# Kernel optimization log

Measured on AMD Instinct MI355X. Metric: run time of the kernel, lower is better.

Reference implementation:

```python
import jax, jax.numpy as jnp
import numpy as np

# MLABlock dims (from __init__ defaults / chosen init_kwargs)
B, S, D = 2, 2048, 2048
H = 16
NOPE, ROPE, VD = 128, 64, 128
KVR = 512
NE, TOPK = 12, 4
EI, SEI = 1024, 2048
THETA = 10000.0
MSCALE = 1.0
EPS = 1e-6


def setup_inputs() -> dict:
    key = jax.random.key(0)
    ks = jax.random.split(key, 14)
    w = lambda k, shp: jax.random.normal(k, shp, jnp.float32) * 0.02
    return {
        "x": jax.random.normal(ks[0], (B, S, D), jnp.float32),
        "start_pos": 0,
        "norm_w": jnp.ones((D,), jnp.float32),
        "wq": w(ks[1], (H * (NOPE + ROPE), D)),
        "wkv_a": w(ks[2], (KVR + ROPE, D)),
        "kv_norm_w": jnp.ones((KVR,), jnp.float32),
        "wkv_b": w(ks[3], (H * (NOPE + VD), KVR)),
        "wo": w(ks[4], (D, H * VD)),
        "gate_w": w(ks[5], (NE, D)),
        "gate_bias": w(ks[6], (NE,)),
        "w1": w(ks[7], (NE, EI, D)),
        "w2": w(ks[8], (NE, D, EI)),
        "w3": w(ks[9], (NE, EI, D)),
        "sw1": w(ks[10], (SEI, D)),
        "sw2": w(ks[11], (D, SEI)),
        "sw3": w(ks[12], (SEI, D)),
    }


def _rms(v, w):
    return v * jax.lax.rsqrt(jnp.mean(v * v, -1, keepdims=True) + EPS) * w


def reference(x, start_pos, norm_w, wq, wkv_a, kv_norm_w, wkv_b, wo,
              gate_w, gate_bias, w1, w2, w3, sw1, sw2, sw3):
    b, s, d = x.shape
    # ---- MLA attention sub-layer ----
    h = _rms(x, norm_w)
    q = (h @ wq.T).reshape(b, s, H, NOPE + ROPE)
    q_nope, q_pe = q[..., :NOPE], q[..., NOPE:]
    kv = h @ wkv_a.T                      # [b,s,KVR+ROPE]
    kv_lat, k_pe = kv[..., :KVR], kv[..., KVR:]
    # rotary embedding (interleaved pairs), positions start_pos..start_pos+s
    pos = jnp.arange(s, dtype=jnp.float32) + start_pos
    inv = 1.0 / (THETA ** (jnp.arange(0, ROPE, 2, dtype=jnp.float32) / ROPE))
    ang = pos[:, None] * inv              # [s, ROPE/2]
    cos = jnp.cos(ang)[None, :, None, :]
    sin = jnp.sin(ang)[None, :, None, :]
    def rot(t):                           # t: [b,s,h,ROPE]
        t1, t2 = t[..., 0::2], t[..., 1::2]
        return jnp.stack([t1 * cos - t2 * sin, t1 * sin + t2 * cos], -1).reshape(t.shape)
    q_pe = rot(q_pe)
    k_pe = rot(k_pe[:, :, None, :])       # [b,s,1,ROPE] shared across heads
    kv_lat = _rms(kv_lat, kv_norm_w)
    kvb = (kv_lat @ wkv_b.T).reshape(b, s, H, NOPE + VD)
    k_nope, v = kvb[..., :NOPE], kvb[..., NOPE:]
    k = jnp.concatenate([k_nope, jnp.broadcast_to(k_pe, (b, s, H, ROPE))], -1)
    qf = jnp.concatenate([q_nope, q_pe], -1)
    scale = MSCALE * (NOPE + ROPE) ** -0.5
    mask = jnp.triu(jnp.full((s, s), -1e9, x.dtype), 1)  # causal
    scores = jnp.einsum('bqhd,bkhd->bhqk', qf, k) * scale + mask
    attn = jax.nn.softmax(scores, -1)
    o = jnp.einsum('bhqk,bkhd->bqhd', attn, v).reshape(b, s, H * VD) @ wo.T
    first = o + x
    # ---- MoE sub-layer (shared self.norm reused) ----
    h2 = _rms(first, norm_w)
    g_scores = jax.nn.sigmoid(h2 @ gate_w.T)             # [b,s,NE]
    _, idx = jax.lax.top_k(g_scores + gate_bias, TOPK)   # adaptive-bias selection
    gw = jnp.take_along_axis(g_scores, idx, -1)          # weights from raw scores
    gw = gw / jnp.sum(gw, -1, keepdims=True)
    out = (jax.nn.silu(h2 @ sw1.T) * (h2 @ sw3.T)) @ sw2.T  # shared expert
    for e in range(NE):                                  # fixed small expert set
        we = jnp.sum(jnp.where(idx == e, gw, 0.0), -1)   # [b,s]
        ye = (jax.nn.silu(h2 @ w1[e].T) * (h2 @ w3[e].T)) @ w2[e].T
        out = out + we[..., None] * ye
    return out + first
```

## Files before the change

kernel.cpp:

```cpp
#include <hip/hip_runtime.h>
#include <cstdint>
#include <cstddef>
#include <cmath>

#define DI __device__ __forceinline__
typedef float f32x4 __attribute__((ext_vector_type(4)));
typedef __bf16 bf16x8 __attribute__((ext_vector_type(8)));
typedef unsigned short u16;
typedef unsigned int u32;

static constexpr int TKN = 4096, SEQ = 2048, DIM = 2048, NH = 16;

DI u16 f2bf(float f) {
  union { float f; u32 u; } v; v.f = f;
  u32 r = v.u + 0x7fffu + ((v.u >> 16) & 1u);
  return (u16)(r >> 16);
}
DI float bf2f(u16 h) {
  union { u32 u; float f; } v; v.u = ((u32)h) << 16;
  return v.f;
}
DI f32x4 mfma16(bf16x8 a, bf16x8 b, f32x4 c) {
  return __builtin_amdgcn_mfma_f32_16x16x32_bf16(a, b, c, 0, 0, 0);
}
DI void gld16(const u16* g, u16* l) {
  __builtin_amdgcn_global_load_lds((const __attribute__((address_space(1))) u32*)g,
                                   (__attribute__((address_space(3))) u32*)l, 16, 0, 0);
}

enum { EF_F32 = 0, EF_BF16 = 1, EF_RES = 2, EF_KV = 3, EF_SILU = 4, EF_ATOM = 5, EF_QROPE = 6 };
enum { AM_DIR = 0, AM_LIST = 1, AM_OFF = 2 };

template<int EPI, int AMODE, int NSEG>
__global__ __launch_bounds__(256)
void gemm_f(const u16* __restrict__ A, const u16* __restrict__ B, void* __restrict__ C,
            int M, int N, int K, size_t apl, size_t bpl,
            const int* __restrict__ list, const int* __restrict__ basep,
            const int* __restrict__ counts,
            const void* __restrict__ aux, const float* __restrict__ gws,
            u16* __restrict__ kd0, u16* __restrict__ kd1, u16* __restrict__ vT,
            const float* __restrict__ cosT)
{
  constexpr int BM = 128, BK = 64;
  __shared__ __align__(16) u16 As[BM * BK];
  __shared__ __align__(16) u16 Bs[BM * BK];
  int rowbase = 0;
  if (AMODE != AM_DIR) {
    int z = blockIdx.z;
    M = counts[z];
    rowbase = basep[z];
    B += (size_t)z * (size_t)N * K;
  }
  int m0 = blockIdx.x * BM, n0 = blockIdx.y * BM;
  if (m0 >= M) return;
  int tid = threadIdx.x, lane = tid & 63, wid = tid >> 6;
  int wm = (wid >> 1) * 64, wn = (wid & 1) * 64;
  int lr = lane & 15, lk = (lane >> 4) * 8;

  const u16* asrc[4];
  const u16* bsrc[4];
  int l8 = lane >> 3, c8 = ((lane & 7) ^ l8) * 8;
  #pragma unroll
  for (int i = 0; i < 4; i++) {
    int chunk = wid * 4 + i;
    int ra = m0 + chunk * 8 + l8;
    size_t rowidx;
    if (AMODE == AM_LIST)      rowidx = (size_t)list[rowbase + (ra < M ? ra : 0)];
    else if (AMODE == AM_OFF)  rowidx = (size_t)(rowbase + (ra < M ? ra : 0));
    else                       rowidx = (size_t)ra;
    asrc[i] = A + rowidx * (size_t)K + c8;
    int rb = n0 + chunk * 8 + l8;
    if (rb >= N) rb = N - 1;
    bsrc[i] = B + (size_t)rb * K + c8;
  }

  f32x4 acc[4][4] = {};
  int sw = lr & 7;
  #pragma unroll 1
  for (int s = 0; s < NSEG; s++) {
    int sa = (s == 4) ? 2 : (s & 1);
    int sb = (s == 5) ? 2 : ((s >> 1) & 1);
    size_t ao = (size_t)sa * apl, bo = (size_t)sb * bpl;
    for (int kt = 0; kt < K; kt += BK) {
      #pragma unroll
      for (int i = 0; i < 4; i++) {
        gld16(asrc[i] + ao + kt, &As[(wid * 4 + i) * 512]);
        gld16(bsrc[i] + bo + kt, &Bs[(wid * 4 + i) * 512]);
      }
      __syncthreads();
      #pragma unroll
      for (int ko = 0; ko < BK; ko += 32) {
        bf16x8 af[4], bv[4];
        int sl = ((((ko + lk) >> 3) ^ sw) << 3);
        #pragma unroll
        for (int i = 0; i < 4; i++)
          af[i] = *(const bf16x8*)(&As[(wm + i * 16 + lr) * 64 + sl]);
        #pragma unroll
        for (int j = 0; j < 4; j++)
          bv[j] = *(const bf16x8*)(&Bs[(wn + j * 16 + lr) * 64 + sl]);
        #pragma unroll
        for (int i = 0; i < 4; i++)
          #pragma unroll
          for (int j = 0; j < 4; j++)
            acc[i][j] = mfma16(af[i], bv[j], acc[i][j]);
      }
      __syncthreads();
    }
  }

  int og = (lane >> 4) * 4;
  if (EPI == EF_KV) {
    if (((n0 >> 7) & 1) == 0) {
      #pragma unroll
      for (int i = 0; i < 4; i++)
        #pragma unroll
        for (int p = 0; p < 4; p++) {
          int r = m0 + wm + i * 16 + og + p;
          #pragma unroll
          for (int j = 0; j < 4; j++) {
            int c = n0 + wn + j * 16 + lr;
            float v = acc[i][j][p];
            int hd = c >> 8, cc = c & 127;
            u16 b0 = f2bf(v);
            u16 b1 = f2bf(v - bf2f(b0));
            size_t base = ((size_t)r * NH + hd) * 128 + cc;
            kd0[base] = b0; kd1[base] = b1;
          }
        }
    } else {
      constexpr size_t VPL = (size_t)32 * 128 * 2048;
      #pragma unroll
      for (int i = 0; i < 4; i++) {
        int r0 = m0 + wm + i * 16 + og;
        int bb = r0 >> 11, ss = r0 & 2047;
        #pragma unroll
        for (int j = 0; j < 4; j++) {
          int c = n0 + wn + j * 16 + lr;
          int hd = c >> 8, ccv = c & 127;
          ushort4 q0, q1, q2;
          #pragma unroll
          for (int p = 0; p < 4; p++) {
            float v = acc[i][j][p];
            u16 b0 = f2bf(v);
            float r1 = v - bf2f(b0);
            u16 b1 = f2bf(r1);
            u16 b2 = f2bf(r1 - bf2f(b1));
            ((u16*)&q0)[p] = b0; ((u16*)&q1)[p] = b1; ((u16*)&q2)[p] = b2;
          }
          size_t vb = ((size_t)((bb * 16 + hd) * 128 + ccv)) * 2048 + ss;
          *(ushort4*)(vT + vb) = q0;
          *(ushort4*)(vT + VPL + vb) = q1;
          *(ushort4*)(vT + 2 * VPL + vb) = q2;
        }
      }
    }
  } else {
    #pragma unroll
    for (int i = 0; i < 4; i++)
      #pragma unroll
      for (int p = 0; p < 4; p++) {
        int r = m0 + wm + i * 16 + og + p;
        if (EPI != EF_QROPE) { if (r >= M) continue; }
        size_t outr = (AMODE == AM_DIR) ? (size_t)r : (size_t)(rowbase + r);
        #pragma unroll
        for (int j = 0; j < 4; j++) {
          int c = n0 + wn + j * 16 + lr;
          float v = acc[i][j][p];
          if (EPI == EF_F32) {
            if (c < N) ((float*)C)[outr * N + c] = v;
          } else if (EPI == EF_BF16) {
            ((u16*)C)[outr * N + c] = f2bf(v);
          } else if (EPI == EF_RES) {
            ((float*)C)[outr * N + c] = v + ((const float*)aux)[outr * N + c];
          } else if (EPI == EF_SILU) {
            float t = bf2f(((const u16*)aux)[outr * N + c]);
            float sg = t / (1.f + __expf(-t));
            ((u16*)C)[outr * N + c] = f2bf(sg * v);
          } else if (EPI == EF_ATOM) {
            int tok = list[outr];
            float w = gws[outr];
            atomicAdd((float*)C + (size_t)tok * N + c, w * v);
          } else if (EPI == EF_QROPE) {
            int wi = c % 192;
            float vo = v;
            if (wi >= 128) {
              float part = __shfl_xor(v, 1);
              int jj = (wi - 128) >> 1;
              int srow = r & (SEQ - 1);
              float cs = cosT[srow * 32 + jj];
              float sn = ((const float*)aux)[srow * 32 + jj];
              vo = (c & 1) ? (part * sn + v * cs) : (v * cs - part * sn);
            }
            u16 b0 = f2bf(vo);
            u16 b1 = f2bf(vo - bf2f(b0));
            kd0[outr * (size_t)N + c] = b0;
            kd1[outr * (size_t)N + c] = b1;
          }
        }
      }
  }
}

__global__ __launch_bounds__(256)
void attn3(const u16* __restrict__ q0p, const u16* __restrict__ q1p,
           const u16* __restrict__ k0p, const u16* __restrict__ k1p,
           const u16* __restrict__ kp0, const u16* __restrict__ kp1,
           const u16* __restrict__ vT, u16* __restrict__ o0, float scale)
{
  constexpr int KLD = 200, VLD = 40, PLD = 36;
  constexpr size_t VPL = (size_t)32 * 128 * 2048;
  constexpr size_t OPL = (size_t)TKN * DIM;
  __shared__ __align__(16) u16 Ks[2][32 * KLD];
  __shared__ __align__(16) u16 Vt[3][128 * VLD];
  __shared__ __align__(16) float Ps[4][16 * PLD];

  int bh = blockIdx.y;
  int b = bh >> 4, h = bh & 15;
  int tid = threadIdx.x, lane = tid & 63, wid = tid >> 6;
  int lr = lane & 15, lg = lane >> 4, lk = lg * 8;
  size_t tbase = (size_t)b * SEQ;
  const u16* vbase = vT + (size_t)bh * 128 * 2048;

  for (int half = 0; half < 2; half++) {
    int qt = half ? (31 - (int)blockIdx.x) : (int)blockIdx.x;
    int q0r = qt * 64;
    bf16x8 qf[2][6];
    {
      size_t qoff = (tbase + q0r + wid * 16 + lr) * (size_t)3072 + h * 192;
      #pragma unroll
      for (int kc = 0; kc < 6; kc++) {
        qf[0][kc] = *(const bf16x8*)(q0p + qoff + kc * 32 + lk);
        qf[1][kc] = *(const bf16x8*)(q1p + qoff + kc * 32 + lk);
      }
    }
    f32x4 oacc[8] = {};
    float mrow[4], lrow[4];
    #pragma unroll
    for (int p = 0; p < 4; p++) { mrow[p] = -1e30f; lrow[p] = 0.f; }

    int nkt = 2 * qt + 2;
    for (int kt = 0; kt < nkt; kt++) {
      __syncthreads();
      int kr0 = kt * 32;
      #pragma unroll
      for (int p = 0; p < 2; p++) {
        const u16* knp = p ? k1p : k0p;
        const u16* kpp = p ? kp1 : kp0;
        #pragma unroll
        for (int i = 0; i < 2; i++) {
          int vv = tid + i * 256, r = vv >> 4, cc8 = (vv & 15) * 8;
          int4 d = *(const int4*)(knp + ((tbase + kr0 + r) * (size_t)NH + h) * 128 + cc8);
          *(int4*)(&Ks[p][r * KLD + cc8]) = d;
        }
        {
          int r = tid >> 3, cc8 = (tid & 7) * 8;
          int4 d = *(const int4*)(kpp + (tbase + kr0 + r) * (size_t)64 + cc8);
          *(int4*)(&Ks[p][r * KLD + 128 + cc8]) = d;
        }
      }
      #pragma unroll
      for (int p = 0; p < 3; p++) {
        #pragma unroll
        for (int i = 0; i < 2; i++) {
          int vv = tid + i * 256, d = vv >> 2, cc8 = (vv & 3) * 8;
          int4 dd = *(const int4*)(vbase + p * VPL + (size_t)d * 2048 + kr0 + cc8);
          *(int4*)(&Vt[p][d * VLD + cc8]) = dd;
        }
      }
      __syncthreads();

      f32x4 sacc[2] = {};
      #pragma unroll
      for (int j = 0; j < 2; j++)
        #pragma unroll
        for (int kc = 0; kc < 6; kc++) {
          bf16x8 kf0 = *(const bf16x8*)(&Ks[0][(j * 16 + lr) * KLD + kc * 32 + lk]);
          bf16x8 kf1 = *(const bf16x8*)(&Ks[1][(j * 16 + lr) * KLD + kc * 32 + lk]);
          f32x4 t = sacc[j];
          t = mfma16(qf[0][kc], kf0, t);
          t = mfma16(qf[1][kc], kf0, t);
          t = mfma16(qf[0][kc], kf1, t);
          sacc[j] = t;
        }

      bool tail = (kt >= 2 * qt);
      float fsc[4];
      #pragma unroll
      for (int p = 0; p < 4; p++) {
        float s0 = sacc[0][p] * scale, s1 = sacc[1][p] * scale;
        if (tail) {
          int qrow = q0r + wid * 16 + lg * 4 + p;
          if (kr0 + lr > qrow) s0 = -1e30f;
          if (kr0 + 16 + lr > qrow) s1 = -1e30f;
        }
        float mx = fmaxf(s0, s1);
        #pragma unroll
        for (int off = 1; off < 16; off <<= 1) mx = fmaxf(mx, __shfl_xor(mx, off));
        float mnew = fmaxf(mrow[p], mx);
        fsc[p] = __expf(mrow[p] - mnew);
        float e0 = __expf(s0 - mnew), e1 = __expf(s1 - mnew);
        float ssum = e0 + e1;
        #pragma unroll
        for (int off = 1; off < 16; off <<= 1) ssum += __shfl_xor(ssum, off);
        lrow[p] = lrow[p] * fsc[p] + ssum;
        mrow[p] = mnew;
        Ps[wid][(lg * 4 + p) * PLD + lr] = e0;
        Ps[wid][(lg * 4 + p) * PLD + 16 + lr] = e1;
      }
      #pragma unroll
      for (int jf = 0; jf < 8; jf++) {
        f32x4 t = oacc[jf];
        t[0] *= fsc[0]; t[1] *= fsc[1]; t[2] *= fsc[2]; t[3] *= fsc[3];
        oacc[jf] = t;
      }

      f32x4 pva = *(const f32x4*)(&Ps[wid][lr * PLD + lk]);
      f32x4 pvb = *(const f32x4*)(&Ps[wid][lr * PLD + lk + 4]);
      union { u16 us[8]; bf16x8 v; } pa0u, pa1u;
      #pragma unroll
      for (int e = 0; e < 4; e++) {
        float va = pva[e];
        u16 b0 = f2bf(va); pa0u.us[e] = b0; pa1u.us[e] = f2bf(va - bf2f(b0));
        float vb = pvb[e];
        u16 c0 = f2bf(vb); pa0u.us[4 + e] = c0; pa1u.us[4 + e] = f2bf(vb - bf2f(c0));
      }

      #pragma unroll
      for (int jf = 0; jf < 8; jf++) {
        bf16x8 vf0 = *(const bf16x8*)(&Vt[0][(jf * 16 + lr) * VLD + lk]);
        bf16x8 vf1 = *(const bf16x8*)(&Vt[1][(jf * 16 + lr) * VLD + lk]);
        bf16x8 vf2 = *(const bf16x8*)(&Vt[2][(jf * 16 + lr) * VLD + lk]);
        f32x4 t = oacc[jf];
        t = mfma16(pa0u.v, vf0, t);
        t = mfma16(pa1u.v, vf0, t);
        t = mfma16(pa0u.v, vf1, t);
        t = mfma16(pa1u.v, vf1, t);
        t = mfma16(pa0u.v, vf2, t);
        oacc[jf] = t;
      }
    }

    #pragma unroll
    for (int p = 0; p < 4; p++) {
      float inv = 1.f / lrow[p];
      int qrow = q0r + wid * 16 + lg * 4 + p;
      size_t base = (tbase + qrow) * (size_t)DIM + h * 128;
      #pragma unroll
      for (int jf = 0; jf < 8; jf++) {
        float val = oacc[jf][p] * inv;
        u16 b0 = f2bf(val);
        float r1 = val - bf2f(b0);
        u16 b1 = f2bf(r1);
        u16 b2 = f2bf(r1 - bf2f(b1));
        size_t idx = base + jf * 16 + lr;
        o0[idx] = b0; o0[OPL + idx] = b1; o0[2 * OPL + idx] = b2;
      }
    }
  }
}

__global__ __launch_bounds__(256)
void rmsnorm3(const float* __restrict__ x, const float* __restrict__ w, u16* __restrict__ out)
{
  __shared__ float sred[4];
  constexpr size_t PL = (size_t)TKN * DIM;
  int t = blockIdx.x, tid = threadIdx.x;
  const float* xp = x + (size_t)t * DIM;
  float vals[8], ss = 0.f;
  #pragma unroll
  for (int i = 0; i < 8; i++) { float v = xp[tid + i * 256]; vals[i] = v; ss += v * v; }
  #pragma unroll
  for (int off = 32; off > 0; off >>= 1) ss += __shfl_xor(ss, off);
  if ((tid & 63) == 0) sred[tid >> 6] = ss;
  __syncthreads();
  ss = sred[0] + sred[1] + sred[2] + sred[3];
  float rstd = 1.f / sqrtf(ss / (float)DIM + 1e-6f);
  #pragma unroll
  for (int i = 0; i < 8; i++) {
    int d = tid + i * 256;
    float v = vals[i] * rstd * w[d];
    u16 b0 = f2bf(v);
    float r1 = v - bf2f(b0);
    u16 b1 = f2bf(r1);
    u16 b2 = f2bf(r1 - bf2f(b1));
    size_t o = (size_t)t * DIM + d;
    out[o] = b0; out[PL + o] = b1; out[2 * PL + o] = b2;
  }
}

__global__ __launch_bounds__(256)
void split3(const float* __restrict__ src, u16* __restrict__ dst, size_t n, size_t pl)
{
  size_t i0 = ((size_t)blockIdx.x * 256 + threadIdx.x) * 4;
  size_t stride = (size_t)gridDim.x * 1024;
  for (size_t i = i0; i < n; i += stride) {
    float4 d = *(const float4*)(src + i);
    ushort4 b0, b1, b2; float r;
    b0.x = f2bf(d.x); r = d.x - bf2f(b0.x); b1.x = f2bf(r); b2.x = f2bf(r - bf2f(b1.x));
    b0.y = f2bf(d.y); r = d.y - bf2f(b0.y); b1.y = f2bf(r); b2.y = f2bf(r - bf2f(b1.y));
    b0.z = f2bf(d.z); r = d.z - bf2f(b0.z); b1.z = f2bf(r); b2.z = f2bf(r - bf2f(b1.z));
    b0.w = f2bf(d.w); r = d.w - bf2f(b0.w); b1.w = f2bf(r); b2.w = f2bf(r - bf2f(b1.w));
    *(ushort4*)(dst + i) = b0;
    *(ushort4*)(dst + pl + i) = b1;
    *(ushort4*)(dst + 2 * pl + i) = b2;
  }
}

__global__ __launch_bounds__(256)
void cvt1(const float* __restrict__ src, u16* __restrict__ dst, size_t n)
{
  size_t i0 = ((size_t)blockIdx.x * 256 + threadIdx.x) * 4;
  size_t stride = (size_t)gridDim.x * 1024;
  for (size_t i = i0; i < n; i += stride) {
    float4 d = *(const float4*)(src + i);
    ushort4 b;
    b.x = f2bf(d.x); b.y = f2bf(d.y); b.z = f2bf(d.z); b.w = f2bf(d.w);
    *(ushort4*)(dst + i) = b;
  }
}

__global__ __launch_bounds__(256)
void kv_split(const float* __restrict__ kvraw, const float* __restrict__ kvw,
              u16* __restrict__ c0, u16* __restrict__ kp0, u16* __restrict__ kp1,
              const float* __restrict__ cosT, const float* __restrict__ sinT)
{
  __shared__ float sred[4];
  constexpr size_t CPL = (size_t)TKN * 512;
  int t = blockIdx.x, tid = threadIdx.x;
  const float* xp = kvraw + (size_t)t * 576;
  float v0 = xp[tid], v1 = xp[tid + 256];
  float ss = v0 * v0 + v1 * v1;
  #pragma unroll
  for (int off = 32; off > 0; off >>= 1) ss += __shfl_xor(ss, off);
  if ((tid & 63) == 0) sred[tid >> 6] = ss;
  __syncthreads();
  ss = sred[0] + sred[1] + sred[2] + sred[3];
  float rstd = 1.f / sqrtf(ss / 512.f + 1e-6f);
  #pragma unroll
  for (int half = 0; half < 2; half++) {
    float v = (half ? v1 : v0) * rstd * kvw[tid + half * 256];
    u16 b0 = f2bf(v);
    float r1 = v - bf2f(b0);
    u16 b1 = f2bf(r1);
    u16 b2 = f2bf(r1 - bf2f(b1));
    size_t o = (size_t)t * 512 + tid + half * 256;
    c0[o] = b0; c0[CPL + o] = b1; c0[2 * CPL + o] = b2;
  }
  if (tid < 32) {
    int srow = t & (SEQ - 1);
    float a = xp[512 + tid * 2], bb = xp[512 + tid * 2 + 1];
    float cs = cosT[srow * 32 + tid], sn = sinT[srow * 32 + tid];
    float ra = a * cs - bb * sn, rb = a * sn + bb * cs;
    u16 a0 = f2bf(ra), a1 = f2bf(ra - bf2f(a0));
    u16 c0b = f2bf(rb), c1 = f2bf(rb - bf2f(c0b));
    kp0[(size_t)t * 64 + tid * 2] = a0;     kp1[(size_t)t * 64 + tid * 2] = a1;
    kp0[(size_t)t * 64 + tid * 2 + 1] = c0b; kp1[(size_t)t * 64 + tid * 2 + 1] = c1;
  }
}

__global__ __launch_bounds__(256)
void rope_table(float* __restrict__ cosT, float* __restrict__ sinT, const int* __restrict__ sp)
{
  int i = blockIdx.x * 256 + threadIdx.x;
  if (i >= SEQ * 32) return;
  int j = i & 31, srow = i >> 5;
  float pos = (float)(srow + sp[0]);
  float inv = powf(10000.f, -(float)(2 * j) / 64.f);
  cosT[i] = cosf(pos * inv);
  sinT[i] = sinf(pos * inv);
}

__global__ __launch_bounds__(256)
void gate_topk(const float* __restrict__ first, const float* __restrict__ nw,
               const float* __restrict__ gwm, const float* __restrict__ gbias,
               int* __restrict__ idx, float* __restrict__ gw4, int* __restrict__ counts,
               u16* __restrict__ h2out)
{
  __shared__ float sred[4];
  __shared__ float sacc[12][4];
  int t = blockIdx.x, tid = threadIdx.x;
  const float* xp = first + (size_t)t * DIM;
  float vals[8], ss = 0.f;
  #pragma unroll
  for (int i = 0; i < 8; i++) { float v = xp[tid + i * 256]; vals[i] = v; ss += v * v; }
  #pragma unroll
  for (int off = 32; off > 0; off >>= 1) ss += __shfl_xor(ss, off);
  if ((tid & 63) == 0) sred[tid >> 6] = ss;
  __syncthreads();
  ss = sred[0] + sred[1] + sred[2] + sred[3];
  float rstd = 1.f / sqrtf(ss / (float)DIM + 1e-6f);
  float acc[12];
  #pragma unroll
  for (int e = 0; e < 12; e++) acc[e] = 0.f;
  #pragma unroll
  for (int i = 0; i < 8; i++) {
    int d = tid + i * 256;
    float v = vals[i] * rstd * nw[d];
    h2out[(size_t)t * DIM + d] = f2bf(v);
    #pragma unroll
    for (int e = 0; e < 12; e++) acc[e] += v * gwm[e * DIM + d];
  }
  #pragma unroll
  for (int e = 0; e < 12; e++) {
    float a = acc[e];
    #pragma unroll
    for (int off = 32; off > 0; off >>= 1) a += __shfl_xor(a, off);
    if ((tid & 63) == 0) sacc[e][tid >> 6] = a;
  }
  __syncthreads();
  if (tid == 0) {
    float g[12], sc[12];
    #pragma unroll
    for (int e = 0; e < 12; e++) {
      float s = sacc[e][0] + sacc[e][1] + sacc[e][2] + sacc[e][3];
      g[e] = 1.f / (1.f + __expf(-s));
      sc[e] = g[e] + gbias[e];
    }
    bool taken[12] = {};
    int sel[4];
    float wsum = 0.f;
    #pragma unroll
    for (int s4 = 0; s4 < 4; s4++) {
      float best = -1e38f; int bi = 0;
      for (int e = 0; e < 12; e++)
        if (!taken[e] && sc[e] > best) { best = sc[e]; bi = e; }
      taken[bi] = true; sel[s4] = bi; wsum += g[bi];
    }
    #pragma unroll
    for (int s4 = 0; s4 < 4; s4++) {
      idx[t * 4 + s4] = sel[s4];
      gw4[t * 4 + s4] = g[sel[s4]] / wsum;
      atomicAdd(&counts[sel[s4]], 1);
    }
  }
}

__global__ void prefix12(const int* __restrict__ counts, int* __restrict__ basep,
                         int* __restrict__ cursor)
{
  if (threadIdx.x == 0) {
    int run = 0;
    for (int e = 0; e < 12; e++) { basep[e] = run; run += counts[e]; cursor[e] = 0; }
  }
}

__global__ __launch_bounds__(256)
void fill_lists(const int* __restrict__ idx, const int* __restrict__ basep,
                int* __restrict__ cursor, int* __restrict__ list,
                const float* __restrict__ gw4, float* __restrict__ gws)
{
  int t = blockIdx.x * 256 + threadIdx.x;
  if (t >= TKN) return;
  #pragma unroll
  for (int s = 0; s < 4; s++) {
    int e = idx[t * 4 + s];
    int pos = atomicAdd(&cursor[e], 1);
    list[basep[e] + pos] = t;
    gws[basep[e] + pos] = gw4[t * 4 + s];
  }
}

extern "C" void kernel_launch(void* const* d_in, const int* in_sizes, int n_in,
                              void* d_out, int out_size, void* d_ws, size_t ws_size,
                              hipStream_t stream)
{
  (void)in_sizes; (void)n_in; (void)out_size; (void)ws_size;
  const float* x      = (const float*)d_in[0];
  const int*   sp     = (const int*)d_in[1];
  const float* norm_w = (const float*)d_in[2];
  const float* wq     = (const float*)d_in[3];
  const float* wkv_a  = (const float*)d_in[4];
  const float* kvnw   = (const float*)d_in[5];
  const float* wkv_b  = (const float*)d_in[6];
  const float* wo     = (const float*)d_in[7];
  const float* gatew  = (const float*)d_in[8];
  const float* gateb  = (const float*)d_in[9];
  const float* w1     = (const float*)d_in[10];
  const float* w2     = (const float*)d_in[11];
  const float* w3     = (const float*)d_in[12];
  const float* sw1    = (const float*)d_in[13];
  const float* sw2    = (const float*)d_in[14];
  const float* sw3    = (const float*)d_in[15];
  float* out = (float*)d_out;
  char* ws = (char*)d_ws;

  const size_t D0 = 0, D1 = 50331648ull, D2 = 100663296ull, D3 = 150994944ull;
  const size_t SM = 188743680ull;
  u16* hpl   = (u16*)(ws + D0);
  u16* cpl   = (u16*)(ws + D0);
  u16* wkvbp = (u16*)(ws + D0 + 12582912ull);
  u16* opl   = (u16*)(ws + D0);
  u16* t1b   = (u16*)(ws + D0);
  u16* asb   = (u16*)(ws + D0 + 16777216ull);
  u16* aeb   = (u16*)(ws + D0);
  u16* qpl   = (u16*)(ws + D1);
  u16* wexp  = (u16*)(ws + D1);
  u16* swp   = (u16*)(ws + D1 + 25165824ull);
  u16* vtp   = (u16*)(ws + D2);
  float* firstb = (float*)(ws + D2);
  u16* h2b   = (u16*)(ws + D2 + 33554432ull);
  u16* wqp   = (u16*)(ws + D3);
  u16* wkvap = (u16*)(ws + D3);
  float* kvr = (float*)(ws + D3 + 7077888ull);
  u16* kpl0  = (u16*)(ws + D3);
  u16* kpl1  = kpl0 + 8388608ull;
  u16* kpe0  = (u16*)(ws + D3 + 33554432ull);
  u16* kpe1  = kpe0 + 262144ull;
  u16* wop   = (u16*)(ws + D3);
  u16* y1eb  = (u16*)(ws + D3);
  float* cosT = (float*)(ws + SM);
  float* sinT = (float*)(ws + SM + 262144ull);
  int*   idxb = (int*)(ws + SM + 524288ull);
  float* gw4b = (float*)(ws + SM + 589824ull);
  int*   listb= (int*)(ws + SM + 655360ull);
  float* gwsb = (float*)(ws + SM + 720896ull);
  int*   cntb = (int*)(ws + SM + 786432ull);
  int*   curb = (int*)(ws + SM + 786688ull);
  int*   baseb= (int*)(ws + SM + 786944ull);

  const size_t PL_TD = (size_t)TKN * DIM;

  hipMemsetAsync(cntb, 0, 256, stream);
  rope_table<<<dim3(256), 256, 0, stream>>>(cosT, sinT, sp);
  rmsnorm3<<<dim3(TKN), 256, 0, stream>>>(x, norm_w, hpl);

  split3<<<dim3(1024), 256, 0, stream>>>(wq, wqp, (size_t)3072 * 2048, 6291456ull);
  gemm_f<EF_QROPE, AM_DIR, 3><<<dim3(32, 24), 256, 0, stream>>>(
      hpl, wqp, nullptr, TKN, 3072, 2048, PL_TD, 6291456ull,
      nullptr, nullptr, nullptr, sinT, nullptr, qpl, qpl + 12582912ull, nullptr, cosT);

  split3<<<dim3(512), 256, 0, stream>>>(wkv_a, wkvap, (size_t)576 * 2048, 1179648ull);
  gemm_f<EF_F32, AM_DIR, 6><<<dim3(32, 5), 256, 0, stream>>>(
      hpl, wkvap, kvr, TKN, 576, 2048, PL_TD, 1179648ull,
      nullptr, nullptr, nullptr, nullptr, nullptr, nullptr, nullptr, nullptr, nullptr);

  kv_split<<<dim3(TKN), 256, 0, stream>>>(kvr, kvnw, cpl, kpe0, kpe1, cosT, sinT);

  split3<<<dim3(1024), 256, 0, stream>>>(wkv_b, wkvbp, (size_t)4096 * 512, 2097152ull);
  gemm_f<EF_KV, AM_DIR, 6><<<dim3(32, 32), 256, 0, stream>>>(
      cpl, wkvbp, nullptr, TKN, 4096, 512, 2097152ull, 2097152ull,
      nullptr, nullptr, nullptr, nullptr, nullptr, kpl0, kpl1, vtp, nullptr);

  attn3<<<dim3(16, 32), 256, 0, stream>>>(qpl, qpl + 12582912ull, kpl0, kpl1,
      kpe0, kpe1, vtp, opl, 1.f / sqrtf(192.f));

  split3<<<dim3(1024), 256, 0, stream>>>(wo, wop, (size_t)2048 * 2048, 4194304ull);
  gemm_f<EF_RES, AM_DIR, 6><<<dim3(32, 16), 256, 0, stream>>>(
      opl, wop, firstb, TKN, 2048, 2048, PL_TD, 4194304ull,
      nullptr, nullptr, nullptr, x, nullptr, nullptr, nullptr, nullptr, nullptr);

  gate_topk<<<dim3(TKN), 256, 0, stream>>>(firstb, norm_w, gatew, gateb, idxb, gw4b, cntb, h2b);
  prefix12<<<dim3(1), 64, 0, stream>>>(cntb, baseb, curb);
  fill_lists<<<dim3(16), 256, 0, stream>>>(idxb, baseb, curb, listb, gw4b, gwsb);

  cvt1<<<dim3(1024), 256, 0, stream>>>(sw1, swp, (size_t)2048 * 2048);
  cvt1<<<dim3(1024), 256, 0, stream>>>(sw3, swp + 4194304ull, (size_t)2048 * 2048);
  cvt1<<<dim3(1024), 256, 0, stream>>>(sw2, swp + 8388608ull, (size_t)2048 * 2048);
  gemm_f<EF_BF16, AM_DIR, 1><<<dim3(32, 16), 256, 0, stream>>>(
      h2b, swp, t1b, TKN, 2048, 2048, 0, 0,
      nullptr, nullptr, nullptr, nullptr, nullptr, nullptr, nullptr, nullptr, nullptr);
  gemm_f<EF_SILU, AM_DIR, 1><<<dim3(32, 16), 256, 0, stream>>>(
      h2b, swp + 4194304ull, asb, TKN, 2048, 2048, 0, 0,
      nullptr, nullptr, nullptr, t1b, nullptr, nullptr, nullptr, nullptr, nullptr);
  gemm_f<EF_RES, AM_DIR, 1><<<dim3(32, 16), 256, 0, stream>>>(
      asb, swp + 8388608ull, out, TKN, 2048, 2048, 0, 0,
      nullptr, nullptr, nullptr, firstb, nullptr, nullptr, nullptr, nullptr, nullptr);

  for (int g = 0; g < 2; g++) {
    cvt1<<<dim3(2048), 256, 0, stream>>>(w1 + (size_t)g * 6 * 1024 * 2048, wexp,
                                         (size_t)6 * 1024 * 2048);
    gemm_f<EF_BF16, AM_LIST, 1><<<dim3(32, 8, 6), 256, 0, stream>>>(
        h2b, wexp, y1eb, 0, 1024, 2048, 0, 0,
        listb, baseb + g * 6, cntb + g * 6, nullptr, nullptr, nullptr, nullptr, nullptr, nullptr);
    cvt1<<<dim3(2048), 256, 0, stream>>>(w3 + (size_t)g * 6 * 1024 * 2048, wexp,
                                         (size_t)6 * 1024 * 2048);
    gemm_f<EF_SILU, AM_LIST, 1><<<dim3(32, 8, 6), 256, 0, stream>>>(
        h2b, wexp, aeb, 0, 1024, 2048, 0, 0,
        listb, baseb + g * 6, cntb + g * 6, y1eb, nullptr, nullptr, nullptr, nullptr, nullptr);
    cvt1<<<dim3(2048), 256, 0, stream>>>(w2 + (size_t)g * 6 * 2048 * 1024, wexp,
                                         (size_t)6 * 2048 * 1024);
    gemm_f<EF_ATOM, AM_OFF, 1><<<dim3(32, 16, 6), 256, 0, stream>>>(
        aeb, wexp, out, 0, 2048, 1024, 0, 0,
        listb, baseb + g * 6, cntb + g * 6, nullptr, gwsb, nullptr, nullptr, nullptr, nullptr);
  }
}
```

Baseline: 2.356 ms.

## Add 256x128-tile double-buffered GEMM for MoE and merge expert launches

Adds a new `gemm8` kernel with 512 threads and 256x128x64 tiles, double-buffered in shared memory and using async global loads with swizzled layout. It replaces the older GEMM for the shared-expert and routed-expert FFN matmuls. The two 6-expert groups are collapsed into single 12-expert launches, each preceded by one full weight conversion. The aim is more operand reuse per tile, fewer launches and better load/compute overlap. In exchange it uses more shared memory per block, which limits occupancy, and it needs the expert weight buffer to hold all 12 experts.

```diff
diff --git a/kernel.cpp b/kernel.cpp
--- a/kernel.cpp
+++ b/kernel.cpp
@@ -201,6 +201,132 @@
   }
 }
 
+template<int EPI, int AMODE>
+__global__ __launch_bounds__(512)
+void gemm8(const u16* __restrict__ A, const u16* __restrict__ B, void* __restrict__ C,
+           int M, int N, int K,
+           const int* __restrict__ list, const int* __restrict__ basep,
+           const int* __restrict__ counts,
+           const void* __restrict__ aux, const float* __restrict__ gws)
+{
+  constexpr int BM = 256, BN = 128, BK = 64;
+  __shared__ __align__(16) u16 As[2][BM * BK];
+  __shared__ __align__(16) u16 Bs[2][BN * BK];
+  int rowbase = 0;
+  if (AMODE != AM_DIR) {
+    int z = blockIdx.z;
+    M = counts[z];
+    rowbase = basep[z];
+    B += (size_t)z * (size_t)N * K;
+  }
+  int m0 = blockIdx.x * BM, n0 = blockIdx.y * BN;
+  if (m0 >= M) return;
+  int tid = threadIdx.x, lane = tid & 63, wid = tid >> 6;
+  int wm = (wid >> 1) * 64, wn = (wid & 1) * 64;
+  int lr = lane & 15, lk = (lane >> 4) * 8;
+
+  const u16* asrc[4];
+  const u16* bsrc[2];
+  int l8 = lane >> 3, c8 = ((lane & 7) ^ l8) * 8;
+  #pragma unroll
+  for (int i = 0; i < 4; i++) {
+    int chunk = wid * 4 + i;
+    int ra = m0 + chunk * 8 + l8;
+    size_t rowidx;
+    if (AMODE == AM_LIST)      rowidx = (size_t)list[rowbase + (ra < M ? ra : 0)];
+    else if (AMODE == AM_OFF)  rowidx = (size_t)(rowbase + (ra < M ? ra : 0));
+    else                       rowidx = (size_t)(ra < M ? ra : 0);
+    asrc[i] = A + rowidx * (size_t)K + c8;
+  }
+  #pragma unroll
+  for (int i = 0; i < 2; i++) {
+    int chunk = wid * 2 + i;
+    int rb = n0 + chunk * 8 + l8;
+    if (rb >= N) rb = N - 1;
+    bsrc[i] = B + (size_t)rb * K + c8;
+  }
+
+  f32x4 acc[4][4] = {};
+  int sw = lr & 7;
+  int nkt = K / BK;
+
+  #pragma unroll
+  for (int i = 0; i < 4; i++) gld16(asrc[i], &As[0][(wid * 4 + i) * 512]);
+  #pragma unroll
+  for (int i = 0; i < 2; i++) gld16(bsrc[i], &Bs[0][(wid * 2 + i) * 512]);
+
+  int cur = 0;
+  for (int kt = 0; kt < nkt; kt++) {
+    int nxt = cur ^ 1;
+    if (kt + 1 < nkt) {
+      int off = (kt + 1) * BK;
+      #pragma unroll
+      for (int i = 0; i < 4; i++) gld16(asrc[i] + off, &As[nxt][(wid * 4 + i) * 512]);
+      #pragma unroll
+      for (int i = 0; i < 2; i++) gld16(bsrc[i] + off, &Bs[nxt][(wid * 2 + i) * 512]);
+      __builtin_amdgcn_sched_barrier(0);
+      asm volatile("s_waitcnt vmcnt(6)" ::: "memory");
+    } else {
+      __builtin_amdgcn_sched_barrier(0);
+      asm volatile("s_waitcnt vmcnt(0)" ::: "memory");
+    }
+    __builtin_amdgcn_sched_barrier(0);
+    __builtin_amdgcn_s_barrier();
+    __builtin_amdgcn_sched_barrier(0);
+    #pragma unroll
+    for (int ko = 0; ko < BK; ko += 32) {
+      bf16x8 af[4], bv[4];
+      int sl = ((((ko + lk) >> 3) ^ sw) << 3);
+      #pragma unroll
+      for (int i = 0; i < 4; i++)
+        af[i] = *(const bf16x8*)(&As[cur][(wm + i * 16 + lr) * 64 + sl]);
+      #pragma unroll
+      for (int j = 0; j < 4; j++)
+        bv[j] = *(const bf16x8*)(&Bs[cur][(wn + j * 16 + lr) * 64 + sl]);
+      __builtin_amdgcn_s_setprio(1);
+      #pragma unroll
+      for (int i = 0; i < 4; i++)
+        #pragma unroll
+        for (int j = 0; j < 4; j++)
+          acc[i][j] = mfma16(af[i], bv[j], acc[i][j]);
+      __builtin_amdgcn_s_setprio(0);
+    }
+    __builtin_amdgcn_sched_barrier(0);
+    __builtin_amdgcn_s_barrier();
+    __builtin_amdgcn_sched_barrier(0);
+    cur = nxt;
+  }
+
+  int og = (lane >> 4) * 4;
+  #pragma unroll
+  for (int i = 0; i < 4; i++)
+    #pragma unroll
+    for (int p = 0; p < 4; p++) {
+      int r = m0 + wm + i * 16 + og + p;
+      if (r >= M) continue;
+      size_t outr = (AMODE == AM_DIR) ? (size_t)r : (size_t)(rowbase + r);
+      #pragma unroll
+      for (int j = 0; j < 4; j++) {
+        int c = n0 + wn + j * 16 + lr;
+        if (c >= N) continue;
+        float v = acc[i][j][p];
+        if (EPI == EF_BF16) {
+          ((u16*)C)[outr * N + c] = f2bf(v);
+        } else if (EPI == EF_RES) {
+          ((float*)C)[outr * N + c] = v + ((const float*)aux)[outr * N + c];
+        } else if (EPI == EF_SILU) {
+          float t = bf2f(((const u16*)aux)[outr * N + c]);
+          float sg = t / (1.f + __expf(-t));
+          ((u16*)C)[outr * N + c] = f2bf(sg * v);
+        } else if (EPI == EF_ATOM) {
+          int tok = list[outr];
+          float w = gws[outr];
+          atomicAdd((float*)C + (size_t)tok * N + c, w * v);
+        }
+      }
+    }
+}
+
 __global__ __launch_bounds__(256)
 void attn3(const u16* __restrict__ q0p, const u16* __restrict__ q1p,
            const u16* __restrict__ k0p, const u16* __restrict__ k1p,
@@ -656,31 +782,20 @@
   cvt1<<<dim3(1024), 256, 0, stream>>>(sw1, swp, (size_t)2048 * 2048);
   cvt1<<<dim3(1024), 256, 0, stream>>>(sw3, swp + 4194304ull, (size_t)2048 * 2048);
   cvt1<<<dim3(1024), 256, 0, stream>>>(sw2, swp + 8388608ull, (size_t)2048 * 2048);
-  gemm_f<EF_BF16, AM_DIR, 1><<<dim3(32, 16), 256, 0, stream>>>(
-      h2b, swp, t1b, TKN, 2048, 2048, 0, 0,
-      nullptr, nullptr, nullptr, nullptr, nullptr, nullptr, nullptr, nullptr, nullptr);
-  gemm_f<EF_SILU, AM_DIR, 1><<<dim3(32, 16), 256, 0, stream>>>(
-      h2b, swp + 4194304ull, asb, TKN, 2048, 2048, 0, 0,
-      nullptr, nullptr, nullptr, t1b, nullptr, nullptr, nullptr, nullptr, nullptr);
-  gemm_f<EF_RES, AM_DIR, 1><<<dim3(32, 16), 256, 0, stream>>>(
-      asb, swp + 8388608ull, out, TKN, 2048, 2048, 0, 0,
-      nullptr, nullptr, nullptr, firstb, nullptr, nullptr, nullptr, nullptr, nullptr);
-
-  for (int g = 0; g < 2; g++) {
-    cvt1<<<dim3(2048), 256, 0, stream>>>(w1 + (size_t)g * 6 * 1024 * 2048, wexp,
-                                         (size_t)6 * 1024 * 2048);
-    gemm_f<EF_BF16, AM_LIST, 1><<<dim3(32, 8, 6), 256, 0, stream>>>(
-        h2b, wexp, y1eb, 0, 1024, 2048, 0, 0,
-        listb, baseb + g * 6, cntb + g * 6, nullptr, nullptr, nullptr, nullptr, nullptr, nullptr);
-    cvt1<<<dim3(2048), 256, 0, stream>>>(w3 + (size_t)g * 6 * 1024 * 2048, wexp,
-                                         (size_t)6 * 1024 * 2048);
-    gemm_f<EF_SILU, AM_LIST, 1><<<dim3(32, 8, 6), 256, 0, stream>>>(
-        h2b, wexp, aeb, 0, 1024, 2048, 0, 0,
-        listb, baseb + g * 6, cntb + g * 6, y1eb, nullptr, nullptr, nullptr, nullptr, nullptr);
-    cvt1<<<dim3(2048), 256, 0, stream>>>(w2 + (size_t)g * 6 * 2048 * 1024, wexp,
-                                         (size_t)6 * 2048 * 1024);
-    gemm_f<EF_ATOM, AM_OFF, 1><<<dim3(32, 16, 6), 256, 0, stream>>>(
-        aeb, wexp, out, 0, 2048, 1024, 0, 0,
-        listb, baseb + g * 6, cntb + g * 6, nullptr, gwsb, nullptr, nullptr, nullptr, nullptr);
-  }
-}
+  gemm8<EF_BF16, AM_DIR><<<dim3(16, 16), 512, 0, stream>>>(
+      h2b, swp, t1b, TKN, 2048, 2048, nullptr, nullptr, nullptr, nullptr, nullptr);
+  gemm8<EF_SILU, AM_DIR><<<dim3(16, 16), 512, 0, stream>>>(
+      h2b, swp + 4194304ull, asb, TKN, 2048, 2048, nullptr, nullptr, nullptr, t1b, nullptr);
+  gemm8<EF_RES, AM_DIR><<<dim3(16, 16), 512, 0, stream>>>(
+      asb, swp + 8388608ull, out, TKN, 2048, 2048, nullptr, nullptr, nullptr, firstb, nullptr);
+
+  cvt1<<<dim3(2048), 256, 0, stream>>>(w1, wexp, (size_t)12 * 1024 * 2048);
+  gemm8<EF_BF16, AM_LIST><<<dim3(16, 8, 12), 512, 0, stream>>>(
+      h2b, wexp, y1eb, 0, 1024, 2048, listb, baseb, cntb, nullptr, nullptr);
+  cvt1<<<dim3(2048), 256, 0, stream>>>(w3, wexp, (size_t)12 * 1024 * 2048);
+  gemm8<EF_SILU, AM_LIST><<<dim3(16, 8, 12), 512, 0, stream>>>(
+      h2b, wexp, aeb, 0, 1024, 2048, listb, baseb, cntb, y1eb, nullptr);
+  cvt1<<<dim3(2048), 256, 0, stream>>>(w2, wexp, (size_t)12 * 2048 * 1024);
+  gemm8<EF_ATOM, AM_OFF><<<dim3(16, 16, 12), 512, 0, stream>>>(
+      aeb, wexp, out, 0, 2048, 1024, listb, baseb, cntb, nullptr, gwsb);
+}
```

Measured after the change: 2.778 ms. +17.9%, slower.
